# Kernel tuning notes

Hardware: AMD Instinct MI355X
Metric: run time of the kernel (lower is better)

Reference implementation:

```python
import jax, jax.numpy as jnp
import numpy as np

ANNEAL = 0.01

def _tsig(x, temp=ANNEAL):
    # temperature sigmoid with +/-50 clipping as in the torch source
    return jax.nn.sigmoid(jnp.clip(x / temp, -50.0, 50.0))

def setup_inputs() -> dict:
    key = jax.random.key(0)
    k1, k2 = jax.random.split(key)
    N, D = 512, 512
    preds = jax.random.normal(k1, (N, D), dtype=jnp.float32)
    labels = jax.random.randint(k2, (N,), 0, 64, dtype=jnp.int64)
    return {"preds": preds, "labels": labels}

def reference(preds, labels):
    N = preds.shape[0]
    dtype = preds.dtype
    eye = jnp.eye(N, dtype=dtype)
    same = (labels[:, None] == labels[None, :]).astype(dtype)
    I_pos = same * (1.0 - eye)                      # positives excl. self
    sim_mat = preds @ preds.T                       # [N, N]
    # sim_diff[i, j, k] = sim_mat[i, k] - sim_mat[i, j]
    sim_sg = _tsig(sim_mat[:, None, :] - sim_mat[:, :, None]) * (1.0 - eye)[None, :, :]
    sim_all_rk = 1.0 + jnp.sum(sim_sg, axis=-1)     # [N, N]
    # sum_k sim_sg[i,j,k] * I_pos[i,k]
    pos_sum = jnp.einsum('ijk,ik->ij', sim_sg, I_pos)
    sim_pos_rk = eye + I_pos + I_pos * pos_sum      # [N, N]
    n_pos = jnp.sum(I_pos, axis=1) + 1.0            # [N]
    per_anchor = jnp.sum(sim_pos_rk / sim_all_rk, axis=1) / n_pos
    per_anchor = jnp.where(n_pos > 1.0, per_anchor, 0.0)  # skip anchors with no positives
    ap = jnp.sum(per_anchor) / N
    return 1.0 - ap
```

## Files before the change

kernel.cpp:

```cpp
#include <hip/hip_runtime.h>

#define NN 512

__global__ __launch_bounds__(512) void sap_fused(const float* __restrict__ P,
                                                 const int* __restrict__ labels,
                                                 float* __restrict__ per_anchor) {
    __shared__ float srow[2][NN];
    __shared__ int   labels_sh[NN];
    __shared__ float posf[NN];
    __shared__ int   poslist[NN];
    __shared__ int   npos_cnt;
    __shared__ float wave_part[8];

    const int t    = threadIdx.x;
    const int lane = t & 63;
    const int wave = t >> 6;
    const int g    = lane & 15;
    const int grp  = lane >> 4;
    const int i0   = blockIdx.x * 2;

    if (t < 128) ((int4*)labels_sh)[t] = ((const int4*)labels)[t];

    float4 a0[8], a1[8];
    {
        const float4* A0 = (const float4*)&P[i0 * NN];
        const float4* A1 = (const float4*)&P[(i0 + 1) * NN];
#pragma unroll
        for (int c = 0; c < 8; ++c) {
            a0[c] = A0[g + 16 * c];
            a1[c] = A1[g + 16 * c];
        }
    }

#pragma unroll 4
    for (int b = 0; b < 16; ++b) {
        const int k = wave * 64 + b * 4 + grp;
        const float4* B = (const float4*)&P[k * NN];
        float s0 = 0.f, s1 = 0.f;
#pragma unroll
        for (int c = 0; c < 8; ++c) {
            const float4 bb = B[g + 16 * c];
            s0 += a0[c].x * bb.x; s0 += a0[c].y * bb.y;
            s0 += a0[c].z * bb.z; s0 += a0[c].w * bb.w;
            s1 += a1[c].x * bb.x; s1 += a1[c].y * bb.y;
            s1 += a1[c].z * bb.z; s1 += a1[c].w * bb.w;
        }
#pragma unroll
        for (int off = 1; off < 16; off <<= 1) {
            s0 += __shfl_xor(s0, off);
            s1 += __shfl_xor(s1, off);
        }
        if (g == 0) { srow[0][k] = s0; srow[1][k] = s1; }
    }

    const float C1   = 100.0f * 1.44269504088896340736f;
    const float CLIP = 50.0f  * 1.44269504088896340736f;

    for (int a = 0; a < 2; ++a) {
        const int i = i0 + a;
        __syncthreads();
        if (t == 0) npos_cnt = 0;
        if (t < 8) wave_part[t] = 0.f;
        __syncthreads();
        const int li = labels_sh[i];
        {
            bool p  = (labels_sh[t] == li) && (t != i);
            posf[t] = p ? 1.f : 0.f;
            if (p) { int idx = atomicAdd(&npos_cnt, 1); poslist[idx] = t; }
        }
        __syncthreads();

        const int cnt = npos_cnt;
        if (cnt == 0) {
            if (t == 0) per_anchor[i] = 0.f;
            continue;
        }

        const float* sr = srow[a];
        float acc = 0.f;
        for (int idx = wave; idx <= cnt; idx += 8) {
            const int   j   = (idx == cnt) ? i : poslist[idx];
            const float sij = sr[j];
            float sum_all = 0.f, sum_pos = 0.f;
#pragma unroll
            for (int kk = 0; kk < 8; kk++) {
                const int k = lane + (kk << 6);
                float y = (sij - sr[k]) * C1;
                y = fminf(fmaxf(y, -CLIP), CLIP);
                float tt = 1.0f / (1.0f + exp2f(y));
                if (k == j) tt = 0.f;
                sum_all += tt;
                sum_pos += tt * posf[k];
            }
#pragma unroll
            for (int off = 32; off; off >>= 1) {
                sum_all += __shfl_down(sum_all, off);
                sum_pos += __shfl_down(sum_pos, off);
            }
            if (lane == 0) {
                const float den = 1.0f + sum_all;
                acc += ((j == i) ? 1.0f : (1.0f + sum_pos)) / den;
            }
        }
        if (lane == 0) wave_part[wave] = acc;
        __syncthreads();
        if (t == 0) {
            float tot = 0.f;
#pragma unroll
            for (int w = 0; w < 8; ++w) tot += wave_part[w];
            per_anchor[i] = tot / (float)(cnt + 1);
        }
    }
}

__global__ __launch_bounds__(256) void sap_reduce(const float* __restrict__ per_anchor,
                                                  float* __restrict__ out) {
    __shared__ float sh[256];
    const int t = threadIdx.x;
    sh[t] = per_anchor[t] + per_anchor[t + 256];
    __syncthreads();
    for (int s = 128; s; s >>= 1) {
        if (t < s) sh[t] += sh[t + s];
        __syncthreads();
    }
    if (t == 0) out[0] = 1.0f - sh[0] / (float)NN;
}

extern "C" void kernel_launch(void* const* d_in, const int* in_sizes, int n_in,
                              void* d_out, int out_size, void* d_ws, size_t ws_size,
                              hipStream_t stream) {
    const float* preds  = (const float*)d_in[0];
    const int*   labels = (const int*)d_in[1];
    float* out        = (float*)d_out;
    float* per_anchor = (float*)d_ws;

    sap_fused<<<NN / 2, 512, 0, stream>>>(preds, labels, per_anchor);
    sap_reduce<<<1, 256, 0, stream>>>(per_anchor, out);
}
```

Baseline: 73.36 us.

## Fuse final reduction into main kernel via inter-block flag spin-wait

Removes the separate reduction kernel launch. Each block publishes its two per-anchor values plus a magic flag with agent-scope atomics, and block 0 spin-waits on all 256 flags before doing the final reduction. This saves a kernel launch and the gap between the two kernels. In exchange it relies on every block making progress while block 0 spins, and block 0 waits on the slowest block.

```diff
diff --git a/kernel.cpp b/kernel.cpp
--- a/kernel.cpp
+++ b/kernel.cpp
@@ -1,23 +1,29 @@
 #include <hip/hip_runtime.h>
 
 #define NN 512
+#define FMAGIC 0x5AD0F1A6u
 
 __global__ __launch_bounds__(512) void sap_fused(const float* __restrict__ P,
                                                  const int* __restrict__ labels,
-                                                 float* __restrict__ per_anchor) {
+                                                 unsigned* __restrict__ pa_bits,
+                                                 unsigned* __restrict__ flags,
+                                                 float* __restrict__ out) {
     __shared__ float srow[2][NN];
     __shared__ int   labels_sh[NN];
     __shared__ float posf[NN];
     __shared__ int   poslist[NN];
     __shared__ int   npos_cnt;
     __shared__ float wave_part[8];
+    __shared__ float pa_out[2];
+    __shared__ float sh[256];
 
     const int t    = threadIdx.x;
     const int lane = t & 63;
     const int wave = t >> 6;
     const int g    = lane & 15;
     const int grp  = lane >> 4;
-    const int i0   = blockIdx.x * 2;
+    const int b    = blockIdx.x;
+    const int i0   = b * 2;
 
     if (t < 128) ((int4*)labels_sh)[t] = ((const int4*)labels)[t];
 
@@ -33,8 +39,8 @@
     }
 
 #pragma unroll 4
-    for (int b = 0; b < 16; ++b) {
-        const int k = wave * 64 + b * 4 + grp;
+    for (int bb_ = 0; bb_ < 16; ++bb_) {
+        const int k = wave * 64 + bb_ * 4 + grp;
         const float4* B = (const float4*)&P[k * NN];
         float s0 = 0.f, s1 = 0.f;
 #pragma unroll
@@ -72,7 +78,7 @@
 
         const int cnt = npos_cnt;
         if (cnt == 0) {
-            if (t == 0) per_anchor[i] = 0.f;
+            if (t == 0) pa_out[a] = 0.f;
             continue;
         }
 
@@ -108,16 +114,39 @@
             float tot = 0.f;
 #pragma unroll
             for (int w = 0; w < 8; ++w) tot += wave_part[w];
-            per_anchor[i] = tot / (float)(cnt + 1);
+            pa_out[a] = tot / (float)(cnt + 1);
         }
     }
-}
+    __syncthreads();
 
-__global__ __launch_bounds__(256) void sap_reduce(const float* __restrict__ per_anchor,
-                                                  float* __restrict__ out) {
-    __shared__ float sh[256];
-    const int t = threadIdx.x;
-    sh[t] = per_anchor[t] + per_anchor[t + 256];
+    if (t == 0) {
+        __hip_atomic_store(&pa_bits[i0],     __float_as_uint(pa_out[0]),
+                           __ATOMIC_RELAXED, __HIP_MEMORY_SCOPE_AGENT);
+        __hip_atomic_store(&pa_bits[i0 + 1], __float_as_uint(pa_out[1]),
+                           __ATOMIC_RELAXED, __HIP_MEMORY_SCOPE_AGENT);
+        asm volatile("s_waitcnt vmcnt(0)" ::: "memory");
+        __hip_atomic_store(&flags[b], FMAGIC,
+                           __ATOMIC_RELAXED, __HIP_MEMORY_SCOPE_AGENT);
+    }
+
+    if (b != 0) return;
+
+    if (t < 256) {
+        while (__hip_atomic_load(&flags[t], __ATOMIC_RELAXED,
+                                 __HIP_MEMORY_SCOPE_AGENT) != FMAGIC)
+            __builtin_amdgcn_s_sleep(8);
+        __hip_atomic_store(&flags[t], 0u, __ATOMIC_RELAXED,
+                           __HIP_MEMORY_SCOPE_AGENT);
+    }
+    __syncthreads();
+
+    if (t < 256) {
+        float v0 = __uint_as_float(__hip_atomic_load(&pa_bits[t], __ATOMIC_RELAXED,
+                                                     __HIP_MEMORY_SCOPE_AGENT));
+        float v1 = __uint_as_float(__hip_atomic_load(&pa_bits[t + 256], __ATOMIC_RELAXED,
+                                                     __HIP_MEMORY_SCOPE_AGENT));
+        sh[t] = v0 + v1;
+    }
     __syncthreads();
     for (int s = 128; s; s >>= 1) {
         if (t < s) sh[t] += sh[t + s];
@@ -131,9 +160,10 @@
                               hipStream_t stream) {
     const float* preds  = (const float*)d_in[0];
     const int*   labels = (const int*)d_in[1];
-    float* out        = (float*)d_out;
-    float* per_anchor = (float*)d_ws;
+    float* out = (float*)d_out;
 
-    sap_fused<<<NN / 2, 512, 0, stream>>>(preds, labels, per_anchor);
-    sap_reduce<<<1, 256, 0, stream>>>(per_anchor, out);
+    unsigned* pa_bits = (unsigned*)d_ws;
+    unsigned* flags   = pa_bits + NN;
+
+    sap_fused<<<NN / 2, 512, 0, stream>>>(preds, labels, pa_bits, flags, out);
 }
```

After: 71.78 us. 2.2% less time.
